# Performance work log

Hardware: AMD Instinct MI355X
Metric: run time of the kernel (lower is better)

## Reference

```python
import jax, jax.numpy as jnp
import numpy as np
from jax import lax

B, P, K = 16, 1024, 32          # clouds, points per cloud, kNN neighbors
N = B * P
NCLS = 40
DIMS = [3, 64, 128, 256]


def setup_inputs() -> dict:
    key = jax.random.key(0)
    ks = jax.random.split(key, 16)
    inp = {
        "x": jax.random.normal(ks[0], (N, DIMS[0]), dtype=jnp.float32),
        "batch": jnp.repeat(jnp.arange(B, dtype=jnp.int64), P),
        "target": jax.random.randint(ks[1], (N,), 0, NCLS, dtype=jnp.int64),
    }
    for i, (fi, fo) in enumerate(zip(DIMS[:-1], DIMS[1:])):
        scale = 1.0 / np.sqrt(2 * fi)
        inp[f"W{i+1}"] = jax.random.normal(ks[2 + 2 * i], (2 * fi, fo), dtype=jnp.float32) * scale
        inp[f"b{i+1}"] = jnp.zeros((fo,), dtype=jnp.float32)
    inp["Wc"] = jax.random.normal(ks[10], (DIMS[-1], NCLS), dtype=jnp.float32) * (1.0 / np.sqrt(DIMS[-1]))
    inp["bc"] = jnp.zeros((NCLS,), dtype=jnp.float32)
    return inp


def knn_graph(x):
    """Per-cloud kNN (loop=False). x: [N,F] with nodes grouped in B clouds of P.
    Returns global neighbor indices [N, K]."""
    xb = x.reshape(B, P, -1)
    sq = jnp.sum(xb * xb, axis=-1)                       # [B,P]
    d2 = sq[:, :, None] + sq[:, None, :] - 2.0 * jnp.einsum("bpf,bqf->bpq", xb, xb)
    d2 = d2 + jnp.eye(P, dtype=x.dtype) * jnp.finfo(x.dtype).max  # exclude self-loops
    _, idx = lax.top_k(-d2, K)                           # [B,P,K] local indices
    gidx = idx + (jnp.arange(B) * P)[:, None, None]      # local -> global node ids
    return gidx.reshape(N, K)


def edge_conv(x, nbr, W, b):
    """EdgeConv: max_j MLP([x_i, x_j - x_i])."""
    xj = x[nbr]                                          # [N,K,F] gather
    xi = x[:, None, :]
    feat = jnp.concatenate([jnp.broadcast_to(xi, xj.shape), xj - xi], axis=-1)  # [N,K,2F]
    h = jnp.einsum("nkf,fo->nko", feat, W) + b           # [N,K,F']
    return jnp.max(h, axis=1)                            # max aggregation


def reference(x, batch, target, W1, b1, W2, b2, W3, b3, Wc, bc):
    del batch  # structure encoded as B clouds of P contiguous nodes
    for W, b in ((W1, b1), (W2, b2), (W3, b3)):
        nbr = knn_graph(x)                               # dynamic graph per layer
        x = jax.nn.relu(edge_conv(x, nbr, W, b))
    logits = x @ Wc + bc                                 # [N, NCLS]
    probs = jax.nn.softmax(logits, axis=-1)
    logp = jax.nn.log_softmax(logits, axis=-1)           # == probs.log()
    loss = -jnp.mean(jnp.take_along_axis(logp, target[:, None], axis=-1))
    return loss, probs
```

## Files before the change

### kernel.cpp

```cpp
#include <hip/hip_runtime.h>
#include <float.h>
#include <math.h>

#define BCLOUDS 16
#define PPTS    1024
#define NPTS    (BCLOUDS * PPTS)
#define KNB     32
#define NCLS    40
#define RPB     4
#define NBIN    256
#define HPADW   (NBIN + NBIN / 16)
#define SELFM   0xFFFFFFFFu

__device__ __forceinline__ int hidx(int b) { return b + (b >> 4); }

template<int F>
__global__ __launch_bounds__(256) void xpose_kernel(const float* __restrict__ x,
                                                    float* __restrict__ xT,
                                                    float* __restrict__ qn) {
    const int p = blockIdx.x * 256 + threadIdx.x;
    const int cloud = p >> 10, pl = p & 1023;
    const float* xr = x + (size_t)p * F;
    float* xTc = xT + (size_t)cloud * F * PPTS;
    float s = 0.f;
    for (int f = 0; f < F; ++f) {
        const float v = xr[f];
        s = fmaf(v, v, s);
        xTc[(size_t)f * PPTS + pl] = v;
    }
    qn[p] = s;
}

template<int F>
__global__ __launch_bounds__(256, 6) void knn_kernel(const float* __restrict__ x,
                                                     const float* __restrict__ xT,
                                                     const float* __restrict__ qn,
                                                     int* __restrict__ nbr) {
    __shared__ unsigned dmat[RPB][PPTS];
    __shared__ float    xp[RPB][F];
    __shared__ float    rn[RPB];
    __shared__ unsigned hist[RPB][HPADW];

    const int tid   = threadIdx.x;
    const int lane  = tid & 63;
    const int wave  = tid >> 6;
    const int bid   = blockIdx.x;
    const int cloud = (bid & 7) + 8 * (bid >> 11);
    const int pl0   = ((bid >> 3) & 255) * RPB;

    const float* xc = x + (size_t)cloud * PPTS * F;
    for (int i = tid; i < RPB * F; i += 256)
        xp[i / F][i % F] = xc[(size_t)(pl0 + i / F) * F + (i % F)];
    __syncthreads();
    if (tid < RPB) {
        float s = 0.f;
        for (int f = 0; f < F; ++f) { const float v = xp[tid][f]; s = fmaf(v, v, s); }
        rn[tid] = s;
    }
    __syncthreads();

    const float* xTc = xT + (size_t)cloud * F * PPTS;
    const float4 qv = *reinterpret_cast<const float4*>(&qn[cloud * PPTS + 4 * tid]);

    float acc[RPB][4];
#pragma unroll
    for (int r = 0; r < RPB; ++r)
#pragma unroll
        for (int c = 0; c < 4; ++c) acc[r][c] = 0.f;

    if constexpr (F % 4 == 0) {
#pragma unroll 2
        for (int f4 = 0; f4 < F / 4; ++f4) {
            float4 vf[4];
#pragma unroll
            for (int j = 0; j < 4; ++j)
                vf[j] = *reinterpret_cast<const float4*>(&xTc[(size_t)(4 * f4 + j) * PPTS + 4 * tid]);
            float4 xr[RPB];
#pragma unroll
            for (int r = 0; r < RPB; ++r) xr[r] = *reinterpret_cast<const float4*>(&xp[r][4 * f4]);
#pragma unroll
            for (int r = 0; r < RPB; ++r) {
                acc[r][0] = fmaf(vf[0].x, xr[r].x, acc[r][0]);
                acc[r][1] = fmaf(vf[0].y, xr[r].x, acc[r][1]);
                acc[r][2] = fmaf(vf[0].z, xr[r].x, acc[r][2]);
                acc[r][3] = fmaf(vf[0].w, xr[r].x, acc[r][3]);
                acc[r][0] = fmaf(vf[1].x, xr[r].y, acc[r][0]);
                acc[r][1] = fmaf(vf[1].y, xr[r].y, acc[r][1]);
                acc[r][2] = fmaf(vf[1].z, xr[r].y, acc[r][2]);
                acc[r][3] = fmaf(vf[1].w, xr[r].y, acc[r][3]);
                acc[r][0] = fmaf(vf[2].x, xr[r].z, acc[r][0]);
                acc[r][1] = fmaf(vf[2].y, xr[r].z, acc[r][1]);
                acc[r][2] = fmaf(vf[2].z, xr[r].z, acc[r][2]);
                acc[r][3] = fmaf(vf[2].w, xr[r].z, acc[r][3]);
                acc[r][0] = fmaf(vf[3].x, xr[r].w, acc[r][0]);
                acc[r][1] = fmaf(vf[3].y, xr[r].w, acc[r][1]);
                acc[r][2] = fmaf(vf[3].z, xr[r].w, acc[r][2]);
                acc[r][3] = fmaf(vf[3].w, xr[r].w, acc[r][3]);
            }
        }
    } else {
        for (int f = 0; f < F; ++f) {
            const float4 v = *reinterpret_cast<const float4*>(&xTc[(size_t)f * PPTS + 4 * tid]);
#pragma unroll
            for (int r = 0; r < RPB; ++r) {
                const float xv = xp[r][f];
                acc[r][0] = fmaf(v.x, xv, acc[r][0]);
                acc[r][1] = fmaf(v.y, xv, acc[r][1]);
                acc[r][2] = fmaf(v.z, xv, acc[r][2]);
                acc[r][3] = fmaf(v.w, xv, acc[r][3]);
            }
        }
    }
#pragma unroll
    for (int r = 0; r < RPB; ++r) {
        uint4 wv;
        float d2;
        d2 = fmaxf(rn[r] + qv.x - 2.f * acc[r][0], 0.f);
        wv.x = (4 * tid + 0 == pl0 + r) ? SELFM : __float_as_uint(d2);
        d2 = fmaxf(rn[r] + qv.y - 2.f * acc[r][1], 0.f);
        wv.y = (4 * tid + 1 == pl0 + r) ? SELFM : __float_as_uint(d2);
        d2 = fmaxf(rn[r] + qv.z - 2.f * acc[r][2], 0.f);
        wv.z = (4 * tid + 2 == pl0 + r) ? SELFM : __float_as_uint(d2);
        d2 = fmaxf(rn[r] + qv.w - 2.f * acc[r][3], 0.f);
        wv.w = (4 * tid + 3 == pl0 + r) ? SELFM : __float_as_uint(d2);
        *reinterpret_cast<uint4*>(&dmat[r][4 * tid]) = wv;
    }
    __syncthreads();

    unsigned* hw = hist[wave];
    const int r = wave;
    unsigned bits[16];
#pragma unroll
    for (int i = 0; i < 16; ++i) bits[i] = dmat[r][lane + i * 64];

    unsigned m = bits[0];
#pragma unroll
    for (int i = 1; i < 16; ++i) m = min(m, bits[i]);
    unsigned gmin = m;
    unsigned tmax = (lane < 32) ? m : 0u;
#pragma unroll
    for (int off = 1; off < 64; off <<= 1) {
        gmin = min(gmin, (unsigned)__shfl_xor((int)gmin, off));
        tmax = max(tmax, (unsigned)__shfl_xor((int)tmax, off));
    }

    unsigned sm = 0u, nam = 0xFFFFu;
    int R = KNB;
    unsigned base = gmin;
    int shift = 0;
    bool do_hist = tmax > gmin;
    if (do_hist) {
        const unsigned span = tmax - gmin;
        const int lg = 31 - __clz(span);
        shift = lg > 7 ? lg - 7 : 0;
    }

#pragma unroll 1
    for (int pass = 0; pass < 2 && do_hist; ++pass) {
        int bin[16];
#pragma unroll
        for (int j = 0; j < 5; ++j) { const int k2 = lane + j * 64; if (k2 < HPADW) hw[k2] = 0u; }
#pragma unroll
        for (int i = 0; i < 16; ++i) {
            if ((nam >> i) & 1) {
                const unsigned d = bits[i] - base;
                int b = (int)(d >> shift);
                b = b > 255 ? 255 : b;
                bin[i] = b;
                atomicAdd(&hw[hidx(b)], 1u);
            } else bin[i] = 256;
        }
        unsigned h[4];
        int cnt = 0;
#pragma unroll
        for (int j = 0; j < 4; ++j) { h[j] = hw[hidx(lane * 4 + j)]; cnt += (int)h[j]; }
        int inc = cnt;
#pragma unroll
        for (int off = 1; off < 64; off <<= 1) {
            const int nv = __shfl_up(inc, off);
            if (lane >= off) inc += nv;
        }
        const int pre = inc - cnt;
        const bool found = (pre < R && R <= inc);
        unsigned pk = 0;
        if (found) {
            int c = pre, bb = -1, cb = 0; unsigned hbv = 0;
#pragma unroll
            for (int j = 0; j < 4; ++j) {
                if (bb < 0) {
                    if (c + (int)h[j] >= R) { bb = lane * 4 + j; hbv = h[j]; cb = c; }
                    else c += (int)h[j];
                }
            }
            pk = (unsigned)bb | ((unsigned)cb << 8) | (hbv << 16);
        }
        const unsigned long long fm = __ballot(found);
        pk = (unsigned)__shfl((int)pk, __ffsll(fm) - 1);
        const int bbin = (int)(pk & 255u);
        const int cb   = (int)((pk >> 8) & 255u);
        const int hb   = (int)(pk >> 16);
        const int need = R - cb;
        unsigned nnam = 0u;
#pragma unroll
        for (int i = 0; i < 16; ++i) {
            if (bin[i] < bbin) sm |= 1u << i;
            else if (bin[i] == bbin) nnam |= 1u << i;
        }
        if (hb == need && bbin != 255) {
            sm |= nnam; R = 0; do_hist = false;
        } else {
            nam = nnam; R = need;
            if (R <= 4 || shift == 0) do_hist = false;
            else {
                base += (unsigned)bbin << shift;
                shift = shift > 8 ? shift - 8 : 0;
            }
        }
    }

#pragma unroll 1
    while (R > 0) {
        unsigned lmin = 0xFFFFFFFFu;
#pragma unroll
        for (int i = 0; i < 16; ++i)
            if ((nam >> i) & 1) lmin = min(lmin, bits[i]);
        unsigned vmin = lmin;
#pragma unroll
        for (int off = 1; off < 64; off <<= 1)
            vmin = min(vmin, (unsigned)__shfl_xor((int)vmin, off));
        unsigned eq = 0u;
#pragma unroll
        for (int i = 0; i < 16; ++i)
            if (((nam >> i) & 1) && bits[i] == vmin) eq |= 1u << i;
        int tot = __popc(eq);
#pragma unroll
        for (int off = 1; off < 64; off <<= 1) tot += __shfl_xor(tot, off);
        if (tot <= R) {
            sm |= eq; nam &= ~eq; R -= tot;
        } else {
#pragma unroll
            for (int i = 0; i < 16; ++i) {
                if (R > 0) {
                    const bool c2 = (eq >> i) & 1;
                    const unsigned long long mb = __ballot(c2);
                    const int t2 = (int)__popcll(mb);
                    if (t2 <= R) { if (c2) sm |= 1u << i; R -= t2; }
                    else {
                        const unsigned long long lower = mb & ((1ull << lane) - 1ull);
                        if (c2 && (int)__popcll(lower) < R) sm |= 1u << i;
                        R = 0;
                    }
                }
            }
        }
    }

    int* out = nbr + (size_t)(cloud * PPTS + pl0 + r) * KNB;
    int tot = 0;
#pragma unroll
    for (int i = 0; i < 16; ++i) {
        const bool c2 = (sm >> i) & 1;
        const unsigned long long mb = __ballot(c2);
        if (c2) {
            const int slot = tot + (int)__popcll(mb & ((1ull << lane) - 1ull));
            if (slot < KNB) out[slot] = cloud * PPTS + lane + i * 64;
        }
        tot += (int)__popcll(mb);
    }
    if (lane == 0)
        for (int s = tot; s < KNB; ++s) out[s] = cloud * PPTS + pl0 + r;
}

template<int F, int FO>
__global__ __launch_bounds__(256) void edge_gemm_kernel(const float* __restrict__ x,
                                                        const float* __restrict__ W,
                                                        const float* __restrict__ bias,
                                                        float* __restrict__ A,
                                                        float* __restrict__ Bm) {
    constexpr int RT  = 16;
    constexpr int RS  = 256 / FO;
    constexpr int RPT = RT / RS;
    __shared__ float xs[RT][F];
    const int tid = threadIdx.x;
    const int n0  = blockIdx.x * RT;
    for (int i = tid; i < RT * F; i += 256)
        xs[i / F][i % F] = x[(size_t)n0 * F + i];
    __syncthreads();

    const int o  = tid % FO;
    const int r0 = tid / FO;
    float accA[RPT], accB[RPT];
#pragma unroll
    for (int i = 0; i < RPT; ++i) { accA[i] = 0.f; accB[i] = 0.f; }

    for (int f = 0; f < F; ++f) {
        const float wt = W[(size_t)f * FO + o];
        const float wb = W[(size_t)(F + f) * FO + o];
        const float wd = wt - wb;
#pragma unroll
        for (int i = 0; i < RPT; ++i) {
            const float xv = xs[r0 + i * RS][f];
            accA[i] = fmaf(xv, wd, accA[i]);
            accB[i] = fmaf(xv, wb, accB[i]);
        }
    }
    const float bo = bias[o];
#pragma unroll
    for (int i = 0; i < RPT; ++i) {
        const size_t row = (size_t)(n0 + r0 + i * RS);
        A[row * FO + o]  = accA[i] + bo;
        Bm[row * FO + o] = accB[i];
    }
}

template<int FO>
__global__ __launch_bounds__(256) void combine_kernel(const float* __restrict__ A,
                                                      const float* __restrict__ Bm,
                                                      const int* __restrict__ nbr,
                                                      float* __restrict__ xout) {
    constexpr int FO4 = FO / 4;
    const int idx = blockIdx.x * 256 + threadIdx.x;
    const int n  = idx / FO4;
    const int o4 = idx % FO4;
    const int* nb = nbr + (size_t)n * KNB;
    const float4* B4 = reinterpret_cast<const float4*>(Bm);
    float4 mx = make_float4(-FLT_MAX, -FLT_MAX, -FLT_MAX, -FLT_MAX);
#pragma unroll 8
    for (int k = 0; k < KNB; ++k) {
        const float4 v = B4[(size_t)nb[k] * FO4 + o4];
        mx.x = fmaxf(mx.x, v.x); mx.y = fmaxf(mx.y, v.y);
        mx.z = fmaxf(mx.z, v.z); mx.w = fmaxf(mx.w, v.w);
    }
    const float4 a = reinterpret_cast<const float4*>(A)[idx];
    float4 rr;
    rr.x = fmaxf(a.x + mx.x, 0.f);
    rr.y = fmaxf(a.y + mx.y, 0.f);
    rr.z = fmaxf(a.z + mx.z, 0.f);
    rr.w = fmaxf(a.w + mx.w, 0.f);
    reinterpret_cast<float4*>(xout)[idx] = rr;
}

__global__ __launch_bounds__(256) void classifier_kernel(const float* __restrict__ x,
                                                         const float* __restrict__ Wc,
                                                         const float* __restrict__ bc,
                                                         const int* __restrict__ target,
                                                         float* __restrict__ probs,
                                                         float* __restrict__ lossbuf) {
    const int tid = threadIdx.x;
    const int lane = tid & 63;
    const int n = blockIdx.x * 4 + (tid >> 6);
    const float* xr = x + (size_t)n * 256;
    float logit = -FLT_MAX;
    if (lane < NCLS) {
        float acc = bc[lane];
        for (int f = 0; f < 256; ++f)
            acc = fmaf(xr[f], Wc[f * NCLS + lane], acc);
        logit = acc;
    }
    float m = logit;
#pragma unroll
    for (int off = 32; off; off >>= 1) m = fmaxf(m, __shfl_xor(m, off));
    const float e = (lane < NCLS) ? __expf(logit - m) : 0.f;
    float s = e;
#pragma unroll
    for (int off = 32; off; off >>= 1) s += __shfl_xor(s, off);
    if (lane < NCLS) probs[(size_t)n * NCLS + lane] = e / s;
    const float lt = __shfl(logit, target[n]);
    if (lane == 0) lossbuf[n] = logf(s) - (lt - m);
}

__global__ __launch_bounds__(256) void loss_reduce_kernel(const float* __restrict__ lossbuf,
                                                          float* __restrict__ out) {
    __shared__ float s[256];
    float acc = 0.f;
    for (int i = threadIdx.x; i < NPTS; i += 256) acc += lossbuf[i];
    s[threadIdx.x] = acc;
    __syncthreads();
    for (int off = 128; off; off >>= 1) {
        if (threadIdx.x < off) s[threadIdx.x] += s[threadIdx.x + off];
        __syncthreads();
    }
    if (threadIdx.x == 0) out[0] = s[0] / (float)NPTS;
}

extern "C" void kernel_launch(void* const* d_in, const int* in_sizes, int n_in,
                              void* d_out, int out_size, void* d_ws, size_t ws_size,
                              hipStream_t stream) {
    (void)in_sizes; (void)n_in; (void)out_size; (void)ws_size;
    const float* x_in   = (const float*)d_in[0];
    const int*   target = (const int*)d_in[2];
    const float* W1 = (const float*)d_in[3];
    const float* b1 = (const float*)d_in[4];
    const float* W2 = (const float*)d_in[5];
    const float* b2 = (const float*)d_in[6];
    const float* W3 = (const float*)d_in[7];
    const float* b3 = (const float*)d_in[8];
    const float* Wc = (const float*)d_in[9];
    const float* bc = (const float*)d_in[10];

    char* ws = (char*)d_ws;
    float* X       = (float*)(ws);
    float* A       = (float*)(ws + (size_t)16 * 1024 * 1024);
    float* Bm      = (float*)(ws + (size_t)32 * 1024 * 1024);
    float* xT      = (float*)(ws + (size_t)32 * 1024 * 1024);
    float* qn      = (float*)(ws + (size_t)40 * 1024 * 1024);
    int*   nbr     = (int*)  (ws + (size_t)48 * 1024 * 1024);
    float* lossbuf = (float*)(ws + (size_t)50 * 1024 * 1024);

    float* outF  = (float*)d_out;
    float* probs = outF + 1;

    xpose_kernel<3><<<NPTS / 256, 256, 0, stream>>>(x_in, xT, qn);
    knn_kernel<3><<<NPTS / RPB, 256, 0, stream>>>(x_in, xT, qn, nbr);
    edge_gemm_kernel<3, 64><<<NPTS / 16, 256, 0, stream>>>(x_in, W1, b1, A, Bm);
    combine_kernel<64><<<NPTS * 16 / 256, 256, 0, stream>>>(A, Bm, nbr, X);

    xpose_kernel<64><<<NPTS / 256, 256, 0, stream>>>(X, xT, qn);
    knn_kernel<64><<<NPTS / RPB, 256, 0, stream>>>(X, xT, qn, nbr);
    edge_gemm_kernel<64, 128><<<NPTS / 16, 256, 0, stream>>>(X, W2, b2, A, Bm);
    combine_kernel<128><<<NPTS * 32 / 256, 256, 0, stream>>>(A, Bm, nbr, X);

    xpose_kernel<128><<<NPTS / 256, 256, 0, stream>>>(X, xT, qn);
    knn_kernel<128><<<NPTS / RPB, 256, 0, stream>>>(X, xT, qn, nbr);
    edge_gemm_kernel<128, 256><<<NPTS / 16, 256, 0, stream>>>(X, W3, b3, A, Bm);
    combine_kernel<256><<<NPTS * 64 / 256, 256, 0, stream>>>(A, Bm, nbr, X);

    classifier_kernel<<<NPTS / 4, 256, 0, stream>>>(X, Wc, bc, target, probs, lossbuf);
    loss_reduce_kernel<<<1, 256, 0, stream>>>(lossbuf, outF);
}
```

Baseline: 396.5 us.

## Split kNN into separate distance and selection kernels via global distance matrix

Replaces the fused kNN kernel, which held a 16KB distance tile in LDS, with a distance kernel that writes the squared-distance matrix to global memory and a selection kernel that runs the histogram top-k from it. Clouds are processed in chunks of 8 so the 32MB matrix fits in the workspace. Column norms are now computed inside the distance kernel instead of by the transpose kernel. The aim is to raise occupancy and let each phase have its own register and LDS budget, at the cost of a round trip through global memory and twice as many launches.

```diff
diff --git a/kernel.cpp b/kernel.cpp
--- a/kernel.cpp
+++ b/kernel.cpp
@@ -8,6 +8,7 @@
 #define KNB     32
 #define NCLS    40
 #define RPB     4
+#define CCH     8
 #define NBIN    256
 #define HPADW   (NBIN + NBIN / 16)
 #define SELFM   0xFFFFFFFFu
@@ -16,37 +17,27 @@
 
 template<int F>
 __global__ __launch_bounds__(256) void xpose_kernel(const float* __restrict__ x,
-                                                    float* __restrict__ xT,
-                                                    float* __restrict__ qn) {
+                                                    float* __restrict__ xT) {
     const int p = blockIdx.x * 256 + threadIdx.x;
     const int cloud = p >> 10, pl = p & 1023;
     const float* xr = x + (size_t)p * F;
     float* xTc = xT + (size_t)cloud * F * PPTS;
-    float s = 0.f;
-    for (int f = 0; f < F; ++f) {
-        const float v = xr[f];
-        s = fmaf(v, v, s);
-        xTc[(size_t)f * PPTS + pl] = v;
-    }
-    qn[p] = s;
+    for (int f = 0; f < F; ++f)
+        xTc[(size_t)f * PPTS + pl] = xr[f];
 }
 
 template<int F>
-__global__ __launch_bounds__(256, 6) void knn_kernel(const float* __restrict__ x,
-                                                     const float* __restrict__ xT,
-                                                     const float* __restrict__ qn,
-                                                     int* __restrict__ nbr) {
-    __shared__ unsigned dmat[RPB][PPTS];
-    __shared__ float    xp[RPB][F];
-    __shared__ float    rn[RPB];
-    __shared__ unsigned hist[RPB][HPADW];
-
-    const int tid   = threadIdx.x;
-    const int lane  = tid & 63;
-    const int wave  = tid >> 6;
-    const int bid   = blockIdx.x;
-    const int cloud = (bid & 7) + 8 * (bid >> 11);
-    const int pl0   = ((bid >> 3) & 255) * RPB;
+__global__ __launch_bounds__(256) void dist_kernel(const float* __restrict__ x,
+                                                   const float* __restrict__ xT,
+                                                   int c0,
+                                                   unsigned* __restrict__ D) {
+    __shared__ float xp[RPB][F];
+    __shared__ float rn[RPB];
+    const int tid = threadIdx.x;
+    const int bid = blockIdx.x;
+    const int cloudrel = bid & 7;
+    const int cloud = c0 + cloudrel;
+    const int pl0 = (bid >> 3) * RPB;
 
     const float* xc = x + (size_t)cloud * PPTS * F;
     for (int i = tid; i < RPB * F; i += 256)
@@ -60,9 +51,8 @@
     __syncthreads();
 
     const float* xTc = xT + (size_t)cloud * F * PPTS;
-    const float4 qv = *reinterpret_cast<const float4*>(&qn[cloud * PPTS + 4 * tid]);
-
     float acc[RPB][4];
+    float qnv[4] = {0.f, 0.f, 0.f, 0.f};
 #pragma unroll
     for (int r = 0; r < RPB; ++r)
 #pragma unroll
@@ -75,6 +65,13 @@
 #pragma unroll
             for (int j = 0; j < 4; ++j)
                 vf[j] = *reinterpret_cast<const float4*>(&xTc[(size_t)(4 * f4 + j) * PPTS + 4 * tid]);
+#pragma unroll
+            for (int j = 0; j < 4; ++j) {
+                qnv[0] = fmaf(vf[j].x, vf[j].x, qnv[0]);
+                qnv[1] = fmaf(vf[j].y, vf[j].y, qnv[1]);
+                qnv[2] = fmaf(vf[j].z, vf[j].z, qnv[2]);
+                qnv[3] = fmaf(vf[j].w, vf[j].w, qnv[3]);
+            }
             float4 xr[RPB];
 #pragma unroll
             for (int r = 0; r < RPB; ++r) xr[r] = *reinterpret_cast<const float4*>(&xp[r][4 * f4]);
@@ -101,6 +98,10 @@
     } else {
         for (int f = 0; f < F; ++f) {
             const float4 v = *reinterpret_cast<const float4*>(&xTc[(size_t)f * PPTS + 4 * tid]);
+            qnv[0] = fmaf(v.x, v.x, qnv[0]);
+            qnv[1] = fmaf(v.y, v.y, qnv[1]);
+            qnv[2] = fmaf(v.z, v.z, qnv[2]);
+            qnv[3] = fmaf(v.w, v.w, qnv[3]);
 #pragma unroll
             for (int r = 0; r < RPB; ++r) {
                 const float xv = xp[r][f];
@@ -113,25 +114,39 @@
     }
 #pragma unroll
     for (int r = 0; r < RPB; ++r) {
+        const int rowrel = (cloudrel << 10) + pl0 + r;
         uint4 wv;
         float d2;
-        d2 = fmaxf(rn[r] + qv.x - 2.f * acc[r][0], 0.f);
+        d2 = fmaxf(rn[r] + qnv[0] - 2.f * acc[r][0], 0.f);
         wv.x = (4 * tid + 0 == pl0 + r) ? SELFM : __float_as_uint(d2);
-        d2 = fmaxf(rn[r] + qv.y - 2.f * acc[r][1], 0.f);
+        d2 = fmaxf(rn[r] + qnv[1] - 2.f * acc[r][1], 0.f);
         wv.y = (4 * tid + 1 == pl0 + r) ? SELFM : __float_as_uint(d2);
-        d2 = fmaxf(rn[r] + qv.z - 2.f * acc[r][2], 0.f);
+        d2 = fmaxf(rn[r] + qnv[2] - 2.f * acc[r][2], 0.f);
         wv.z = (4 * tid + 2 == pl0 + r) ? SELFM : __float_as_uint(d2);
-        d2 = fmaxf(rn[r] + qv.w - 2.f * acc[r][3], 0.f);
+        d2 = fmaxf(rn[r] + qnv[3] - 2.f * acc[r][3], 0.f);
         wv.w = (4 * tid + 3 == pl0 + r) ? SELFM : __float_as_uint(d2);
-        *reinterpret_cast<uint4*>(&dmat[r][4 * tid]) = wv;
-    }
-    __syncthreads();
-
+        *reinterpret_cast<uint4*>(&D[(size_t)rowrel * PPTS + 4 * tid]) = wv;
+    }
+}
+
+__global__ __launch_bounds__(256) void select_kernel(const unsigned* __restrict__ D,
+                                                     int c0,
+                                                     int* __restrict__ nbr) {
+    __shared__ unsigned hist[4][HPADW];
+    const int tid = threadIdx.x;
+    const int lane = tid & 63;
+    const int wave = tid >> 6;
+    const int bid = blockIdx.x;
+    const int cloudrel = bid & 7;
+    const int cloud = c0 + cloudrel;
+    const int p = ((bid >> 3) & 255) * 4 + wave;
+    const int rowrel = (cloudrel << 10) + p;
+    const unsigned* Drow = D + (size_t)rowrel * PPTS;
     unsigned* hw = hist[wave];
-    const int r = wave;
+
     unsigned bits[16];
 #pragma unroll
-    for (int i = 0; i < 16; ++i) bits[i] = dmat[r][lane + i * 64];
+    for (int i = 0; i < 16; ++i) bits[i] = Drow[lane + i * 64];
 
     unsigned m = bits[0];
 #pragma unroll
@@ -255,7 +270,7 @@
         }
     }
 
-    int* out = nbr + (size_t)(cloud * PPTS + pl0 + r) * KNB;
+    int* out = nbr + (size_t)(cloud * PPTS + p) * KNB;
     int tot = 0;
 #pragma unroll
     for (int i = 0; i < 16; ++i) {
@@ -268,7 +283,7 @@
         tot += (int)__popcll(mb);
     }
     if (lane == 0)
-        for (int s = tot; s < KNB; ++s) out[s] = cloud * PPTS + pl0 + r;
+        for (int s = tot; s < KNB; ++s) out[s] = cloud * PPTS + p;
 }
 
 template<int F, int FO>
@@ -399,29 +414,38 @@
     const float* bc = (const float*)d_in[10];
 
     char* ws = (char*)d_ws;
-    float* X       = (float*)(ws);
-    float* A       = (float*)(ws + (size_t)16 * 1024 * 1024);
-    float* Bm      = (float*)(ws + (size_t)32 * 1024 * 1024);
-    float* xT      = (float*)(ws + (size_t)32 * 1024 * 1024);
-    float* qn      = (float*)(ws + (size_t)40 * 1024 * 1024);
-    int*   nbr     = (int*)  (ws + (size_t)48 * 1024 * 1024);
-    float* lossbuf = (float*)(ws + (size_t)50 * 1024 * 1024);
+    float*    X       = (float*)(ws);
+    float*    xT      = (float*)(ws + (size_t)8  * 1024 * 1024);
+    unsigned* Dm      = (unsigned*)(ws + (size_t)16 * 1024 * 1024);
+    float*    A       = (float*)(ws + (size_t)16 * 1024 * 1024);
+    float*    Bm      = (float*)(ws + (size_t)32 * 1024 * 1024);
+    int*      nbr     = (int*)  (ws + (size_t)48 * 1024 * 1024);
+    float*    lossbuf = (float*)(ws + (size_t)50 * 1024 * 1024);
 
     float* outF  = (float*)d_out;
     float* probs = outF + 1;
 
-    xpose_kernel<3><<<NPTS / 256, 256, 0, stream>>>(x_in, xT, qn);
-    knn_kernel<3><<<NPTS / RPB, 256, 0, stream>>>(x_in, xT, qn, nbr);
+    xpose_kernel<3><<<NPTS / 256, 256, 0, stream>>>(x_in, xT);
+    for (int c0 = 0; c0 < BCLOUDS; c0 += CCH) {
+        dist_kernel<3><<<CCH * PPTS / RPB, 256, 0, stream>>>(x_in, xT, c0, Dm);
+        select_kernel<<<CCH * PPTS / RPB, 256, 0, stream>>>(Dm, c0, nbr);
+    }
     edge_gemm_kernel<3, 64><<<NPTS / 16, 256, 0, stream>>>(x_in, W1, b1, A, Bm);
     combine_kernel<64><<<NPTS * 16 / 256, 256, 0, stream>>>(A, Bm, nbr, X);
 
-    xpose_kernel<64><<<NPTS / 256, 256, 0, stream>>>(X, xT, qn);
-    knn_kernel<64><<<NPTS / RPB, 256, 0, stream>>>(X, xT, qn, nbr);
+    xpose_kernel<64><<<NPTS / 256, 256, 0, stream>>>(X, xT);
+    for (int c0 = 0; c0 < BCLOUDS; c0 += CCH) {
+        dist_kernel<64><<<CCH * PPTS / RPB, 256, 0, stream>>>(X, xT, c0, Dm);
+        select_kernel<<<CCH * PPTS / RPB, 256, 0, stream>>>(Dm, c0, nbr);
+    }
     edge_gemm_kernel<64, 128><<<NPTS / 16, 256, 0, stream>>>(X, W2, b2, A, Bm);
     combine_kernel<128><<<NPTS * 32 / 256, 256, 0, stream>>>(A, Bm, nbr, X);
 
-    xpose_kernel<128><<<NPTS / 256, 256, 0, stream>>>(X, xT, qn);
-    knn_kernel<128><<<NPTS / RPB, 256, 0, stream>>>(X, xT, qn, nbr);
+    xpose_kernel<128><<<NPTS / 256, 256, 0, stream>>>(X, xT);
+    for (int c0 = 0; c0 < BCLOUDS; c0 += CCH) {
+        dist_kernel<128><<<CCH * PPTS / RPB, 256, 0, stream>>>(X, xT, c0, Dm);
+        select_kernel<<<CCH * PPTS / RPB, 256, 0, stream>>>(Dm, c0, nbr);
+    }
     edge_gemm_kernel<128, 256><<<NPTS / 16, 256, 0, stream>>>(X, W3, b3, A, Bm);
     combine_kernel<256><<<NPTS * 64 / 256, 256, 0, stream>>>(A, Bm, nbr, X);
 
```

Measured after the change: 485.4 us. +22.4%, slower.
